# Kernel optimization log

Hardware: AMD Instinct MI355X
Metric: run time of the kernel (lower is better)

Reference implementation:

```python
import jax, jax.numpy as jnp
import numpy as np

N, E, G = 50000, 800000, 512
IN_DIM, EDGE_DIM, HID, OUT_DIM, HEADS = 16, 8, 32, 64, 4
NEG_SLOPE = 0.2


def _glorot(key, shape):
    fan_in, fan_out = shape[0], shape[-1]
    lim = jnp.sqrt(6.0 / (fan_in + fan_out))
    return jax.random.uniform(key, shape, jnp.float32, -lim, lim)


def setup_inputs() -> dict:
    key = jax.random.key(0)
    ks = jax.random.split(key, 32)
    inp = {
        "x": jax.random.normal(ks[0], (N, IN_DIM), jnp.float32),
        "edge_src": jax.random.randint(ks[1], (E,), 0, N, jnp.int32),
        "edge_dst": jax.random.randint(ks[2], (E,), 0, N, jnp.int32),
        "edge_attr": jax.random.normal(ks[3], (E, EDGE_DIM), jnp.float32),
        "batch": jnp.sort(jax.random.randint(ks[4], (N,), 0, G, jnp.int32)),
    }
    # layer 1: in=16 -> heads=4, C=32
    inp["W1s"] = _glorot(ks[5], (IN_DIM, HEADS * HID)); inp["W1d"] = _glorot(ks[6], (IN_DIM, HEADS * HID))
    inp["W1e"] = _glorot(ks[7], (EDGE_DIM, HEADS * HID))
    inp["b1s"] = jnp.zeros((HEADS * HID,)); inp["b1d"] = jnp.zeros((HEADS * HID,))
    inp["att1"] = _glorot(ks[8], (HEADS, HID)); inp["bias1"] = jnp.zeros((HEADS * HID,))
    # layer 2: in=128 -> heads=4, C=32
    D2 = HEADS * HID
    inp["W2s"] = _glorot(ks[9], (D2, HEADS * HID)); inp["W2d"] = _glorot(ks[10], (D2, HEADS * HID))
    inp["W2e"] = _glorot(ks[11], (EDGE_DIM, HEADS * HID))
    inp["b2s"] = jnp.zeros((HEADS * HID,)); inp["b2d"] = jnp.zeros((HEADS * HID,))
    inp["att2"] = _glorot(ks[12], (HEADS, HID)); inp["bias2"] = jnp.zeros((HEADS * HID,))
    # layer 3: in=128 -> heads=1, C=32
    inp["W3s"] = _glorot(ks[13], (D2, HID)); inp["W3d"] = _glorot(ks[14], (D2, HID))
    inp["W3e"] = _glorot(ks[15], (EDGE_DIM, HID))
    inp["b3s"] = jnp.zeros((HID,)); inp["b3d"] = jnp.zeros((HID,))
    inp["att3"] = _glorot(ks[16], (1, HID)); inp["bias3"] = jnp.zeros((HID,))
    # MLP: 32 -> 64 -> 64
    inp["Wm1"] = _glorot(ks[17], (HID, 2 * HID)); inp["bm1"] = jnp.zeros((2 * HID,))
    inp["Wm2"] = _glorot(ks[18], (2 * HID, OUT_DIM)); inp["bm2"] = jnp.zeros((OUT_DIM,))
    return inp


def gatv2_conv(x, src, dst, edge_attr, Ws, Wd, We, bs, bd, att, bias, heads, ch):
    n = x.shape[0]
    xs = (x @ Ws + bs).reshape(n, heads, ch)   # lin_l (source / value)
    xd = (x @ Wd + bd).reshape(n, heads, ch)   # lin_r (target)
    ea = (edge_attr @ We).reshape(-1, heads, ch)
    z = jax.nn.leaky_relu(xs[src] + xd[dst] + ea, NEG_SLOPE)       # [E,H,C]
    e = jnp.einsum('ehc,hc->eh', z, att)                           # [E,H]
    m = jax.ops.segment_max(e, dst, num_segments=n)                # scatter-softmax over dst
    p = jnp.exp(e - m[dst])
    denom = jax.ops.segment_sum(p, dst, num_segments=n)
    alpha = p / denom[dst]                                          # [E,H]
    msg = xs[src] * alpha[:, :, None]                               # [E,H,C]
    out = jax.ops.segment_sum(msg, dst, num_segments=n)
    return out.reshape(n, heads * ch) + bias


def reference(x, edge_src, edge_dst, edge_attr, batch,
              W1s, W1d, W1e, b1s, b1d, att1, bias1,
              W2s, W2d, W2e, b2s, b2d, att2, bias2,
              W3s, W3d, W3e, b3s, b3d, att3, bias3,
              Wm1, bm1, Wm2, bm2):
    h = jax.nn.elu(gatv2_conv(x, edge_src, edge_dst, edge_attr, W1s, W1d, W1e, b1s, b1d, att1, bias1, HEADS, HID))
    h = jax.nn.elu(gatv2_conv(h, edge_src, edge_dst, edge_attr, W2s, W2d, W2e, b2s, b2d, att2, bias2, HEADS, HID))
    h = gatv2_conv(h, edge_src, edge_dst, edge_attr, W3s, W3d, W3e, b3s, b3d, att3, bias3, 1, HID)
    # global mean pool over graphs
    sums = jax.ops.segment_sum(h, batch, num_segments=G)
    cnt = jax.ops.segment_sum(jnp.ones((h.shape[0],), h.dtype), batch, num_segments=G)
    emb = sums / jnp.maximum(cnt, 1.0)[:, None]
    return jax.nn.relu(emb @ Wm1 + bm1) @ Wm2 + bm2
```

## Files before the change

### kernel.cpp

```cpp
#include <hip/hip_runtime.h>
#include <cstdint>
#include <cstddef>

constexpr int kN = 50000;
constexpr int kE = 800000;
constexpr int kG = 512;
constexpr float kNegSlope = 0.2f;

typedef float f4v __attribute__((ext_vector_type(4)));
typedef _Float16 h2v __attribute__((ext_vector_type(2)));
typedef _Float16 h4v __attribute__((ext_vector_type(4)));
typedef _Float16 h8v __attribute__((ext_vector_type(8)));

#if defined(__has_builtin)
#if __has_builtin(__builtin_amdgcn_fdot2)
#define HAS_FDOT2 1
#endif
#endif

__device__ inline float dot2f(h2v a, h2v b, float c) {
#ifdef HAS_FDOT2
  return __builtin_amdgcn_fdot2(a, b, c, false);
#else
  return c + (float)a.x * (float)b.x + (float)a.y * (float)b.y;
#endif
}

__global__ void k_hist(const int* __restrict__ dst, int* __restrict__ counts,
                       int* __restrict__ pos, int n) {
  int i = blockIdx.x * blockDim.x + threadIdx.x;
  if (i < n) pos[i] = atomicAdd(&counts[dst[i]], 1);
}

__global__ __launch_bounds__(256) void k_scan_blk(const int* __restrict__ counts,
                                                  int* __restrict__ excl,
                                                  int* __restrict__ bsums, int n) {
  __shared__ int sh[256];
  int tid = threadIdx.x;
  int i = blockIdx.x * 256 + tid;
  int c = (i < n) ? counts[i] : 0;
  sh[tid] = c;
  __syncthreads();
  for (int off = 1; off < 256; off <<= 1) {
    int t = (tid >= off) ? sh[tid - off] : 0;
    __syncthreads();
    sh[tid] += t;
    __syncthreads();
  }
  if (i < n) excl[i] = sh[tid] - c;
  if (tid == 255) bsums[blockIdx.x] = sh[255];
}

__global__ __launch_bounds__(256) void k_scan_add(const int* __restrict__ excl,
                                                  const int* __restrict__ bsums,
                                                  int* __restrict__ row_ptr,
                                                  int n, int nb) {
  __shared__ int sh[256];
  int tid = threadIdx.x;
  int c = (tid < nb) ? bsums[tid] : 0;
  sh[tid] = c;
  __syncthreads();
  for (int off = 1; off < 256; off <<= 1) {
    int t = (tid >= off) ? sh[tid - off] : 0;
    __syncthreads();
    sh[tid] += t;
    __syncthreads();
  }
  int top = (blockIdx.x > 0) ? sh[blockIdx.x - 1] : 0;
  int total = sh[nb - 1];
  __syncthreads();
  int i = blockIdx.x * 256 + tid;
  if (i < n) row_ptr[i] = excl[i] + top;
  if (i == n) row_ptr[n] = total;
}

__global__ void k_scatter(const int* __restrict__ src, const int* __restrict__ dst,
                          const float* __restrict__ eattr,
                          const int* __restrict__ row_ptr, const int* __restrict__ pos,
                          uint16_t* __restrict__ csr_src, _Float16* __restrict__ csr_ea,
                          int n) {
  int i = blockIdx.x * blockDim.x + threadIdx.x;
  if (i >= n) return;
  int p = row_ptr[dst[i]] + pos[i];
  csr_src[p] = (uint16_t)src[i];
  const float4* s4 = (const float4*)eattr + (size_t)i * 2;
  float4 a = s4[0];
  float4 b = s4[1];
  h8v hv;
  hv[0] = (_Float16)a.x; hv[1] = (_Float16)a.y; hv[2] = (_Float16)a.z; hv[3] = (_Float16)a.w;
  hv[4] = (_Float16)b.x; hv[5] = (_Float16)b.y; hv[6] = (_Float16)b.z; hv[7] = (_Float16)b.w;
  *(h8v*)(csr_ea + (size_t)p * 8) = hv;
}

__global__ __launch_bounds__(256) void k_prep(
    const float* __restrict__ x,
    const float* __restrict__ W1s, const float* __restrict__ W1d,
    const float* __restrict__ W2s, const float* __restrict__ W2d,
    const float* __restrict__ W3s, const float* __restrict__ W3d,
    const float* __restrict__ W1e, const float* __restrict__ W2e,
    const float* __restrict__ W3e,
    int* __restrict__ counts,
    _Float16* __restrict__ xf, _Float16* __restrict__ Wt1,
    _Float16* __restrict__ Wt2, _Float16* __restrict__ Wt3,
    _Float16* __restrict__ We1t, _Float16* __restrict__ We2t,
    _Float16* __restrict__ We3t, int n) {
  int i = blockIdx.x * 256 + threadIdx.x;
  if (i < n) {
    counts[i] = 0;
  }
  i -= n;
  if (i < 0) return;
  int r0 = n * 32;
  if (i < r0) {
    int node = i >> 5, col = i & 31;
    xf[i] = (col < 16) ? (_Float16)x[node * 16 + col] : (_Float16)0.f;
    return;
  }
  i -= r0;
  if (i < 256 * 32) {
    int c = i >> 5, k = i & 31;
    const float* W = (c < 128) ? W1s : W1d;
    Wt1[i] = (k < 16) ? (_Float16)W[k * 128 + (c & 127)] : (_Float16)0.f;
    return;
  }
  i -= 256 * 32;
  if (i < 256 * 128) {
    int c = i >> 7, k = i & 127;
    const float* W = (c < 128) ? W2s : W2d;
    Wt2[i] = (_Float16)W[k * 128 + (c & 127)];
    return;
  }
  i -= 256 * 128;
  if (i < 64 * 128) {
    int c = i >> 7, k = i & 127;
    const float* W = (c < 32) ? W3s : W3d;
    int cc = (c < 32) ? c : c - 32;
    Wt3[i] = (_Float16)W[k * 32 + cc];
    return;
  }
  i -= 64 * 128;
  if (i < 128 * 8) {
    We1t[i] = (_Float16)W1e[(i & 7) * 128 + (i >> 3)];
    return;
  }
  i -= 128 * 8;
  if (i < 128 * 8) {
    We2t[i] = (_Float16)W2e[(i & 7) * 128 + (i >> 3)];
    return;
  }
  i -= 128 * 8;
  if (i < 32 * 8) {
    We3t[i] = (_Float16)W3e[(i & 7) * 32 + (i >> 3)];
  }
}

template <int KT, int NC2>
__global__ __launch_bounds__(256) void k_tmfma(
    const _Float16* __restrict__ hf, const _Float16* __restrict__ Wt,
    const float* __restrict__ bs, const float* __restrict__ bd,
    _Float16* __restrict__ xs_h, _Float16* __restrict__ xd_h, int n_nodes) {
  constexpr int K = KT * 32;
  constexpr int NCS = NC2 / 2;
  constexpr int D = NCS * 16;
  int lane = threadIdx.x & 63;
  int wid = threadIdx.x >> 6;
  int m = lane & 15;
  int quad = lane >> 4;
  int base = (blockIdx.x * 4 + wid) * 16;
  if (base >= n_nodes) return;
  int arow = min(base + m, n_nodes - 1);

  h8v a[KT];
#pragma unroll
  for (int t = 0; t < KT; ++t)
    a[t] = *(const h8v*)(hf + (size_t)arow * K + t * 32 + quad * 8);

  bool full = (base + 16 <= n_nodes);
#pragma unroll
  for (int c = 0; c < NC2; ++c) {
    f4v acc = {0.f, 0.f, 0.f, 0.f};
#pragma unroll
    for (int t = 0; t < KT; ++t) {
      h8v b = *(const h8v*)(Wt + (size_t)(c * 16 + m) * K + t * 32 + quad * 8);
      acc = __builtin_amdgcn_mfma_f32_16x16x32_f16(a[t], b, acc, 0, 0, 0);
    }
    float bv = (c < NCS) ? bs[c * 16 + m] : bd[(c - NCS) * 16 + m];
#pragma unroll
    for (int r = 0; r < 4; ++r) {
      int node = base + quad * 4 + r;
      if (full || node < n_nodes) {
        if (c < NCS)
          xs_h[(size_t)node * D + c * 16 + m] = (_Float16)(acc[r] + bv);
        else
          xd_h[(size_t)node * D + (c - NCS) * 16 + m] = (_Float16)(acc[r] + bv);
      }
    }
  }
}

template <bool DO_ELU>
__global__ __launch_bounds__(64) void k_gat128(
    const int* __restrict__ row_ptr, const uint16_t* __restrict__ csr_src,
    const _Float16* __restrict__ csr_ea,
    const _Float16* __restrict__ xs_h, const _Float16* __restrict__ xd_h,
    const float* __restrict__ att, const float* __restrict__ bias,
    const _Float16* __restrict__ Wet, _Float16* __restrict__ hout, int n_nodes) {
  __shared__ _Float16 sea[64 * 8];
  int lane = threadIdx.x & 63;
  int node = blockIdx.x;
  if (node >= n_nodes) return;
  int slot = lane >> 5;
  int sl = lane & 31;
  int ch0 = sl * 4;

  float4 at4 = *(const float4*)(att + ch0);
  float atl[4] = {at4.x, at4.y, at4.z, at4.w};
  h2v we[4][4];
#pragma unroll
  for (int c = 0; c < 4; ++c) {
    h8v wv = *(const h8v*)(Wet + (size_t)(ch0 + c) * 8);
#pragma unroll
    for (int t = 0; t < 4; ++t) {
      h2v w;
      w[0] = wv[2 * t];
      w[1] = wv[2 * t + 1];
      we[c][t] = w;
    }
  }
  float4 bv4 = *(const float4*)(bias + ch0);
  float bl[4] = {bv4.x, bv4.y, bv4.z, bv4.w};

  h4v xdh = *(const h4v*)(xd_h + (size_t)node * 128 + ch0);
  float xdl[4];
#pragma unroll
  for (int c = 0; c < 4; ++c) xdl[c] = (float)xdh[c];

  const char* xsb = (const char*)xs_h;
  uint32_t chb = (uint32_t)sl * 8u;

  float acc[4] = {0.f, 0.f, 0.f, 0.f};
  float l_run = 0.f;
  int beg = row_ptr[node], end = row_ptr[node + 1];

  for (int cbeg = beg; cbeg < end; cbeg += 64) {
    int cnt = min(end - cbeg, 64);
    int sv = (lane < cnt) ? (int)__builtin_nontemporal_load(csr_src + cbeg + lane) : 0;
    if (lane < cnt) {
      h8v t = __builtin_nontemporal_load((const h8v*)(csr_ea + (size_t)(cbeg + lane) * 8));
      *(h8v*)&sea[lane * 8] = t;
    }

    auto addr = [&](int i) -> uint32_t {
      int s = __shfl(sv, i + slot, 64);
      return (uint32_t)s * 256u + chb;
    };
    auto consume = [&](int i, h4v xh) {
      int e = i + slot;
      const h2v* pe = (const h2v*)&sea[e * 8];
      h2v a0 = pe[0], a1 = pe[1], a2 = pe[2], a3 = pe[3];
      float xf[4];
#pragma unroll
      for (int c = 0; c < 4; ++c) xf[c] = (float)xh[c];
      float sc = 0.f;
#pragma unroll
      for (int c = 0; c < 4; ++c) {
        float z = dot2f(a3, we[c][3],
                  dot2f(a2, we[c][2],
                  dot2f(a1, we[c][1],
                  dot2f(a0, we[c][0], xf[c] + xdl[c]))));
        z = fmaxf(z, kNegSlope * z);
        sc = fmaf(z, atl[c], sc);
      }
      sc += __shfl_xor(sc, 1, 64);
      sc += __shfl_xor(sc, 2, 64);
      sc += __shfl_xor(sc, 4, 64);
      float p = (e < cnt) ? __expf(sc) : 0.f;
      l_run += p;
#pragma unroll
      for (int c = 0; c < 4; ++c) acc[c] += p * xf[c];
    };

    uint32_t oa = addr(0), ob = addr(2);
    h4v xa = *(const h4v*)(xsb + oa);
    h4v xb = *(const h4v*)(xsb + ob);
    for (int i = 0; i < cnt; i += 4) {
      bool pf = (i + 4 < cnt);
      h4v pa, pb;
      if (pf) {
        uint32_t na = addr(i + 4), nb = addr(i + 6);
        pa = *(const h4v*)(xsb + na);
        pb = *(const h4v*)(xsb + nb);
      }
      consume(i, xa);
      consume(i + 2, xb);
      if (pf) { xa = pa; xb = pb; }
    }
  }

  l_run += __shfl_xor(l_run, 32, 64);
#pragma unroll
  for (int c = 0; c < 4; ++c) acc[c] += __shfl_xor(acc[c], 32, 64);

  if (slot == 0) {
    float inv = (l_run > 0.f) ? (1.f / l_run) : 0.f;
    h4v ov;
#pragma unroll
    for (int c = 0; c < 4; ++c) {
      float o = acc[c] * inv + bl[c];
      if (DO_ELU) o = (o > 0.f) ? o : (__expf(o) - 1.f);
      ov[c] = (_Float16)o;
    }
    __builtin_nontemporal_store(ov, (h4v*)(hout + (size_t)node * 128 + ch0));
  }
}

template <bool DO_ELU>
__global__ __launch_bounds__(64) void k_gat32(
    const int* __restrict__ row_ptr, const uint16_t* __restrict__ csr_src,
    const _Float16* __restrict__ csr_ea,
    const _Float16* __restrict__ xs_h, const _Float16* __restrict__ xd_h,
    const float* __restrict__ att, const float* __restrict__ bias,
    const _Float16* __restrict__ Wet, _Float16* __restrict__ hout, int n_nodes) {
  __shared__ _Float16 sea[32 * 8];
  int lane = threadIdx.x & 63;
  int node = blockIdx.x;
  if (node >= n_nodes) return;
  int slot = lane >> 3;
  int sl = lane & 7;
  int ch0 = sl * 4;

  float4 at4 = *(const float4*)(att + ch0);
  float atl[4] = {at4.x, at4.y, at4.z, at4.w};
  h2v we[4][4];
#pragma unroll
  for (int c = 0; c < 4; ++c) {
    h8v wv = *(const h8v*)(Wet + (size_t)(ch0 + c) * 8);
#pragma unroll
    for (int t = 0; t < 4; ++t) {
      h2v w;
      w[0] = wv[2 * t];
      w[1] = wv[2 * t + 1];
      we[c][t] = w;
    }
  }
  float4 bv4 = *(const float4*)(bias + ch0);
  float bl[4] = {bv4.x, bv4.y, bv4.z, bv4.w};

  h4v xdh = *(const h4v*)(xd_h + (size_t)node * 32 + ch0);
  float xdl[4];
#pragma unroll
  for (int c = 0; c < 4; ++c) xdl[c] = (float)xdh[c];

  const char* xsb = (const char*)xs_h;
  uint32_t chb = (uint32_t)sl * 8u;

  float acc[4] = {0.f, 0.f, 0.f, 0.f};
  float l_run = 0.f;
  int beg = row_ptr[node], end = row_ptr[node + 1];

  for (int cbeg = beg; cbeg < end; cbeg += 32) {
    int cnt = min(end - cbeg, 32);
    int sv = (lane < cnt) ? (int)__builtin_nontemporal_load(csr_src + cbeg + lane) : 0;
    if (lane < cnt) {
      h8v t = __builtin_nontemporal_load((const h8v*)(csr_ea + (size_t)(cbeg + lane) * 8));
      *(h8v*)&sea[lane * 8] = t;
    }

    auto addr = [&](int i) -> uint32_t {
      int idx = (i + slot) & 31;
      int s = __shfl(sv, idx, 64);
      return (uint32_t)s * 64u + chb;
    };
    auto consume = [&](int i, h4v xh) {
      int e = i + slot;
      const h2v* pe = (const h2v*)&sea[e * 8];
      h2v a0 = pe[0], a1 = pe[1], a2 = pe[2], a3 = pe[3];
      float xf[4];
#pragma unroll
      for (int c = 0; c < 4; ++c) xf[c] = (float)xh[c];
      float sc = 0.f;
#pragma unroll
      for (int c = 0; c < 4; ++c) {
        float z = dot2f(a3, we[c][3],
                  dot2f(a2, we[c][2],
                  dot2f(a1, we[c][1],
                  dot2f(a0, we[c][0], xf[c] + xdl[c]))));
        z = fmaxf(z, kNegSlope * z);
        sc = fmaf(z, atl[c], sc);
      }
      sc += __shfl_xor(sc, 1, 64);
      sc += __shfl_xor(sc, 2, 64);
      sc += __shfl_xor(sc, 4, 64);
      float p = (e < cnt) ? __expf(sc) : 0.f;
      l_run += p;
#pragma unroll
      for (int c = 0; c < 4; ++c) acc[c] += p * xf[c];
    };

    uint32_t oa = addr(0), ob = addr(8);
    h4v xa = *(const h4v*)(xsb + oa);
    h4v xb = *(const h4v*)(xsb + ob);
    for (int i = 0; i < cnt; i += 16) {
      bool pf = (i + 16 < cnt);
      h4v pa, pb;
      if (pf) {
        uint32_t na = addr(i + 16), nb = addr(i + 24);
        pa = *(const h4v*)(xsb + na);
        pb = *(const h4v*)(xsb + nb);
      }
      consume(i, xa);
      consume(i + 8, xb);
      if (pf) { xa = pa; xb = pb; }
    }
  }

#pragma unroll
  for (int off = 8; off < 64; off <<= 1) {
    l_run += __shfl_xor(l_run, off, 64);
#pragma unroll
    for (int c = 0; c < 4; ++c) acc[c] += __shfl_xor(acc[c], off, 64);
  }

  if (slot == 0) {
    float inv = (l_run > 0.f) ? (1.f / l_run) : 0.f;
    h4v ov;
#pragma unroll
    for (int c = 0; c < 4; ++c) {
      float o = acc[c] * inv + bl[c];
      if (DO_ELU) o = (o > 0.f) ? o : (__expf(o) - 1.f);
      ov[c] = (_Float16)o;
    }
    __builtin_nontemporal_store(ov, (h4v*)(hout + (size_t)node * 32 + ch0));
  }
}

__device__ inline int lowerb(const int* a, int n, int v) {
  int lo = 0, hi = n;
  while (lo < hi) {
    int mid = (lo + hi) >> 1;
    if (a[mid] < v) lo = mid + 1; else hi = mid;
  }
  return lo;
}

__global__ __launch_bounds__(64) void k_pool_mlp(
    const _Float16* __restrict__ h3, const int* __restrict__ batch,
    const float* __restrict__ Wm1, const float* __restrict__ bm1,
    const float* __restrict__ Wm2, const float* __restrict__ bm2,
    float* __restrict__ out, int n_nodes) {
  int g = blockIdx.x;
  int t = threadIdx.x;
  int lo = lowerb(batch, n_nodes, g);
  int hi = lowerb(batch, n_nodes, g + 1);
  int c = t & 31, half = t >> 5;
  float sum = 0.f;
  for (int i = lo + half; i < hi; i += 2) sum += (float)h3[(size_t)i * 32 + c];
  sum += __shfl_xor(sum, 32, 64);
  float cnt = (float)(hi - lo);
  float emb = sum / fmaxf(cnt, 1.f);
  __shared__ float sh_emb[32];
  __shared__ float sh_hid[64];
  if (half == 0) sh_emb[c] = emb;
  __syncthreads();
  float hv = bm1[t];
  for (int k = 0; k < 32; ++k) hv += sh_emb[k] * Wm1[k * 64 + t];
  hv = fmaxf(hv, 0.f);
  sh_hid[t] = hv;
  __syncthreads();
  float ov = bm2[t];
  for (int k = 0; k < 64; ++k) ov += sh_hid[k] * Wm2[k * 64 + t];
  out[(size_t)g * 64 + t] = ov;
}

extern "C" void kernel_launch(void* const* d_in, const int* in_sizes, int n_in,
                              void* d_out, int out_size, void* d_ws, size_t ws_size,
                              hipStream_t stream) {
  const float* x = (const float*)d_in[0];
  const int* esrc = (const int*)d_in[1];
  const int* edst = (const int*)d_in[2];
  const float* eattr = (const float*)d_in[3];
  const int* batch = (const int*)d_in[4];
  const float* W1s = (const float*)d_in[5];
  const float* W1d = (const float*)d_in[6];
  const float* W1e = (const float*)d_in[7];
  const float* b1s = (const float*)d_in[8];
  const float* b1d = (const float*)d_in[9];
  const float* att1 = (const float*)d_in[10];
  const float* bias1 = (const float*)d_in[11];
  const float* W2s = (const float*)d_in[12];
  const float* W2d = (const float*)d_in[13];
  const float* W2e = (const float*)d_in[14];
  const float* b2s = (const float*)d_in[15];
  const float* b2d = (const float*)d_in[16];
  const float* att2 = (const float*)d_in[17];
  const float* bias2 = (const float*)d_in[18];
  const float* W3s = (const float*)d_in[19];
  const float* W3d = (const float*)d_in[20];
  const float* W3e = (const float*)d_in[21];
  const float* b3s = (const float*)d_in[22];
  const float* b3d = (const float*)d_in[23];
  const float* att3 = (const float*)d_in[24];
  const float* bias3 = (const float*)d_in[25];
  const float* Wm1 = (const float*)d_in[26];
  const float* bm1 = (const float*)d_in[27];
  const float* Wm2 = (const float*)d_in[28];
  const float* bm2 = (const float*)d_in[29];

  constexpr int kNB = (kN + 255) / 256;

  char* p = (char*)d_ws;
  auto take = [&](size_t bytes) {
    char* r = p;
    p += (bytes + 255) & ~(size_t)255;
    return r;
  };
  int* row_ptr = (int*)take((size_t)(kN + 1) * sizeof(int));
  int* counts = (int*)take((size_t)kN * sizeof(int));
  int* pos = (int*)take((size_t)kE * sizeof(int));
  int* excl = (int*)take((size_t)kN * sizeof(int));
  int* bsums = (int*)take((size_t)kNB * sizeof(int));
  uint16_t* csr_src = (uint16_t*)take((size_t)kE * sizeof(uint16_t));
  _Float16* csr_ea = (_Float16*)take((size_t)kE * 8 * sizeof(_Float16));
  _Float16* xf = (_Float16*)take((size_t)kN * 32 * sizeof(_Float16));
  _Float16* Wt1 = (_Float16*)take((size_t)256 * 32 * sizeof(_Float16));
  _Float16* Wt2 = (_Float16*)take((size_t)256 * 128 * sizeof(_Float16));
  _Float16* Wt3 = (_Float16*)take((size_t)64 * 128 * sizeof(_Float16));
  _Float16* We1t = (_Float16*)take((size_t)128 * 8 * sizeof(_Float16));
  _Float16* We2t = (_Float16*)take((size_t)128 * 8 * sizeof(_Float16));
  _Float16* We3t = (_Float16*)take((size_t)32 * 8 * sizeof(_Float16));
  _Float16* xs_h = (_Float16*)take((size_t)kN * 128 * sizeof(_Float16));
  _Float16* xd_h = (_Float16*)take((size_t)kN * 128 * sizeof(_Float16));
  _Float16* hA = (_Float16*)take((size_t)kN * 128 * sizeof(_Float16));
  _Float16* hB = (_Float16*)take((size_t)kN * 128 * sizeof(_Float16));
  _Float16* h3 = (_Float16*)take((size_t)kN * 32 * sizeof(_Float16));

  {
    int prep_total = kN + kN * 32 + 256 * 32 + 256 * 128 + 64 * 128 +
                     128 * 8 + 128 * 8 + 32 * 8;
    k_prep<<<(prep_total + 255) / 256, 256, 0, stream>>>(
        x, W1s, W1d, W2s, W2d, W3s, W3d, W1e, W2e, W3e,
        counts, xf, Wt1, Wt2, Wt3, We1t, We2t, We3t, kN);
  }
  k_hist<<<(kE + 255) / 256, 256, 0, stream>>>(edst, counts, pos, kE);
  k_scan_blk<<<kNB, 256, 0, stream>>>(counts, excl, bsums, kN);
  k_scan_add<<<(kN + 1 + 255) / 256, 256, 0, stream>>>(excl, bsums, row_ptr, kN, kNB);
  k_scatter<<<(kE + 255) / 256, 256, 0, stream>>>(esrc, edst, eattr, row_ptr, pos,
                                                  csr_src, csr_ea, kE);

  constexpr int kTB = (kN + 63) / 64;

  k_tmfma<1, 16><<<kTB, 256, 0, stream>>>(xf, Wt1, b1s, b1d, xs_h, xd_h, kN);
  k_gat128<true><<<kN, 64, 0, stream>>>(row_ptr, csr_src, csr_ea, xs_h, xd_h,
                                        att1, bias1, We1t, hA, kN);
  k_tmfma<4, 16><<<kTB, 256, 0, stream>>>(hA, Wt2, b2s, b2d, xs_h, xd_h, kN);
  k_gat128<true><<<kN, 64, 0, stream>>>(row_ptr, csr_src, csr_ea, xs_h, xd_h,
                                        att2, bias2, We2t, hB, kN);
  k_tmfma<4, 4><<<kTB, 256, 0, stream>>>(hB, Wt3, b3s, b3d, xs_h, xd_h, kN);
  k_gat32<false><<<kN, 64, 0, stream>>>(row_ptr, csr_src, csr_ea, xs_h, xd_h,
                                        att3, bias3, We3t, h3, kN);
  k_pool_mlp<<<kG, 64, 0, stream>>>(h3, batch, Wm1, bm1, Wm2, bm2, (float*)d_out, kN);
}
```

Before: 429.5 us.

## Process two nodes per GAT block with prefetched edges, DPP reductions, exp2

Each GAT aggregation block now handles two destination nodes and loads both nodes' first edge chunks up front, so the second node's edge loads overlap the first node's work. Source addresses are staged in LDS instead of being broadcast with shuffles. The score reduction uses DPP adds, and exp is computed as exp2 with log2e folded into the attention vector. Graph offsets for pooling are built in the prep kernel instead of by binary search. Processing the two nodes one after the other inside a block adds latency per block and may lower occupancy through higher register use.

```diff
diff --git a/kernel.cpp b/kernel.cpp
--- a/kernel.cpp
+++ b/kernel.cpp
@@ -6,6 +6,7 @@
 constexpr int kE = 800000;
 constexpr int kG = 512;
 constexpr float kNegSlope = 0.2f;
+constexpr float kLog2e = 1.4426950408889634f;
 
 typedef float f4v __attribute__((ext_vector_type(4)));
 typedef _Float16 h2v __attribute__((ext_vector_type(2)));
@@ -24,6 +25,13 @@
 #else
   return c + (float)a.x * (float)b.x + (float)a.y * (float)b.y;
 #endif
+}
+
+template <int CTRL>
+__device__ inline float dpp_xadd(float x) {
+  int s = __builtin_bit_cast(int, x);
+  int y = __builtin_amdgcn_update_dpp(s, s, CTRL, 0xF, 0xF, false);
+  return x + __builtin_bit_cast(float, y);
 }
 
 __global__ void k_hist(const int* __restrict__ dst, int* __restrict__ counts,
@@ -99,6 +107,7 @@
     const float* __restrict__ W3s, const float* __restrict__ W3d,
     const float* __restrict__ W1e, const float* __restrict__ W2e,
     const float* __restrict__ W3e,
+    const int* __restrict__ batch, int* __restrict__ gptr,
     int* __restrict__ counts,
     _Float16* __restrict__ xf, _Float16* __restrict__ Wt1,
     _Float16* __restrict__ Wt2, _Float16* __restrict__ Wt3,
@@ -107,6 +116,12 @@
   int i = blockIdx.x * 256 + threadIdx.x;
   if (i < n) {
     counts[i] = 0;
+    int b1 = batch[i];
+    int b0 = (i == 0) ? -1 : batch[i - 1];
+    for (int g = b0 + 1; g <= b1; ++g) gptr[g] = i;
+    if (i == n - 1) {
+      for (int g = b1 + 1; g <= kG; ++g) gptr[g] = n;
+    }
   }
   i -= n;
   if (i < 0) return;
@@ -199,22 +214,49 @@
 }
 
 template <bool DO_ELU>
-__global__ __launch_bounds__(64) void k_gat128(
+__global__ __launch_bounds__(64, 8) void k_gat128(
     const int* __restrict__ row_ptr, const uint16_t* __restrict__ csr_src,
     const _Float16* __restrict__ csr_ea,
     const _Float16* __restrict__ xs_h, const _Float16* __restrict__ xd_h,
     const float* __restrict__ att, const float* __restrict__ bias,
     const _Float16* __restrict__ Wet, _Float16* __restrict__ hout, int n_nodes) {
   __shared__ _Float16 sea[64 * 8];
+  __shared__ uint32_t sad[64];
   int lane = threadIdx.x & 63;
-  int node = blockIdx.x;
-  if (node >= n_nodes) return;
+  int node0 = blockIdx.x * 2;
+  if (node0 >= n_nodes) return;
   int slot = lane >> 5;
   int sl = lane & 31;
   int ch0 = sl * 4;
 
+  int nd1 = min(node0 + 1, n_nodes - 1);
+  int beg0 = row_ptr[node0];
+  int mid = row_ptr[node0 + 1];
+  int end1 = row_ptr[nd1 + 1];
+
+  int cnt0 = min(mid - beg0, 64);
+  int sv0 = 0;
+  h8v ea0;
+#pragma unroll
+  for (int q = 0; q < 8; ++q) ea0[q] = (_Float16)0.f;
+  if (cnt0 > 0) {
+    int idx = beg0 + ((lane < cnt0) ? lane : 0);
+    sv0 = (int)__builtin_nontemporal_load(csr_src + idx);
+    ea0 = __builtin_nontemporal_load((const h8v*)(csr_ea + (size_t)idx * 8));
+  }
+  int pcnt = (node0 + 1 < n_nodes) ? min(end1 - mid, 64) : 0;
+  int sv1 = 0;
+  h8v ea1;
+#pragma unroll
+  for (int q = 0; q < 8; ++q) ea1[q] = (_Float16)0.f;
+  if (pcnt > 0) {
+    int idx = mid + ((lane < pcnt) ? lane : 0);
+    sv1 = (int)__builtin_nontemporal_load(csr_src + idx);
+    ea1 = __builtin_nontemporal_load((const h8v*)(csr_ea + (size_t)idx * 8));
+  }
+
   float4 at4 = *(const float4*)(att + ch0);
-  float atl[4] = {at4.x, at4.y, at4.z, at4.w};
+  float atl[4] = {at4.x * kLog2e, at4.y * kLog2e, at4.z * kLog2e, at4.w * kLog2e};
   h2v we[4][4];
 #pragma unroll
   for (int c = 0; c < 4; ++c) {
@@ -229,108 +271,142 @@
   }
   float4 bv4 = *(const float4*)(bias + ch0);
   float bl[4] = {bv4.x, bv4.y, bv4.z, bv4.w};
-
-  h4v xdh = *(const h4v*)(xd_h + (size_t)node * 128 + ch0);
-  float xdl[4];
-#pragma unroll
-  for (int c = 0; c < 4; ++c) xdl[c] = (float)xdh[c];
+  h4v xdh0 = *(const h4v*)(xd_h + (size_t)node0 * 128 + ch0);
+  h4v xdh1 = *(const h4v*)(xd_h + (size_t)nd1 * 128 + ch0);
 
   const char* xsb = (const char*)xs_h;
   uint32_t chb = (uint32_t)sl * 8u;
-
-  float acc[4] = {0.f, 0.f, 0.f, 0.f};
-  float l_run = 0.f;
-  int beg = row_ptr[node], end = row_ptr[node + 1];
-
-  for (int cbeg = beg; cbeg < end; cbeg += 64) {
-    int cnt = min(end - cbeg, 64);
-    int sv = (lane < cnt) ? (int)__builtin_nontemporal_load(csr_src + cbeg + lane) : 0;
-    if (lane < cnt) {
-      h8v t = __builtin_nontemporal_load((const h8v*)(csr_ea + (size_t)(cbeg + lane) * 8));
-      *(h8v*)&sea[lane * 8] = t;
-    }
-
-    auto addr = [&](int i) -> uint32_t {
-      int s = __shfl(sv, i + slot, 64);
-      return (uint32_t)s * 256u + chb;
-    };
-    auto consume = [&](int i, h4v xh) {
-      int e = i + slot;
-      const h2v* pe = (const h2v*)&sea[e * 8];
-      h2v a0 = pe[0], a1 = pe[1], a2 = pe[2], a3 = pe[3];
-      float xf[4];
-#pragma unroll
-      for (int c = 0; c < 4; ++c) xf[c] = (float)xh[c];
-      float sc = 0.f;
+  const uint32_t* sp = &sad[slot];
+
+  auto run_node = [&](int node, int beg, int end, h4v xdh, int psv, h8v pea) {
+    float xdl[4];
+#pragma unroll
+    for (int c = 0; c < 4; ++c) xdl[c] = (float)xdh[c];
+    float acc[4] = {0.f, 0.f, 0.f, 0.f};
+    float l_run = 0.f;
+    for (int cbeg = beg; cbeg < end; cbeg += 64) {
+      int cnt = min(end - cbeg, 64);
+      int sv;
+      h8v ev;
+      if (cbeg == beg) {
+        sv = psv;
+        ev = pea;
+      } else {
+        int idx = cbeg + ((lane < cnt) ? lane : 0);
+        sv = (int)__builtin_nontemporal_load(csr_src + idx);
+        ev = __builtin_nontemporal_load((const h8v*)(csr_ea + (size_t)idx * 8));
+      }
+      sad[lane] = (lane < cnt) ? ((uint32_t)(uint16_t)sv << 8) : 0u;
+      *(h8v*)&sea[lane * 8] = ev;
+
+      auto consume = [&](int i, h4v xh) {
+        int e = i + slot;
+        const h2v* pe = (const h2v*)&sea[e * 8];
+        h2v a0 = pe[0], a1 = pe[1], a2 = pe[2], a3 = pe[3];
+        float xf[4];
+#pragma unroll
+        for (int c = 0; c < 4; ++c) xf[c] = (float)xh[c];
+        float sc = 0.f;
+#pragma unroll
+        for (int c = 0; c < 4; ++c) {
+          float z = dot2f(a3, we[c][3],
+                    dot2f(a2, we[c][2],
+                    dot2f(a1, we[c][1],
+                    dot2f(a0, we[c][0], xf[c] + xdl[c]))));
+          z = fmaxf(z, kNegSlope * z);
+          sc = fmaf(z, atl[c], sc);
+        }
+        sc = dpp_xadd<0xB1>(sc);
+        sc = dpp_xadd<0x4E>(sc);
+        sc = dpp_xadd<0x141>(sc);
+        float p = (e < cnt) ? exp2f(sc) : 0.f;
+        l_run += p;
+#pragma unroll
+        for (int c = 0; c < 4; ++c) acc[c] += p * xf[c];
+      };
+
+      uint32_t oa = sp[0] + chb, ob = sp[2] + chb;
+      h4v xa = *(const h4v*)(xsb + oa);
+      h4v xb = *(const h4v*)(xsb + ob);
+      for (int i = 0; i < cnt; i += 4) {
+        bool pf = (i + 4 < cnt);
+        h4v pa, pb;
+        if (pf) {
+          uint32_t na = sp[i + 4] + chb, nb = sp[i + 6] + chb;
+          pa = *(const h4v*)(xsb + na);
+          pb = *(const h4v*)(xsb + nb);
+        }
+        consume(i, xa);
+        consume(i + 2, xb);
+        if (pf) { xa = pa; xb = pb; }
+      }
+    }
+
+    l_run += __shfl_xor(l_run, 32, 64);
+#pragma unroll
+    for (int c = 0; c < 4; ++c) acc[c] += __shfl_xor(acc[c], 32, 64);
+
+    if (slot == 0) {
+      float inv = (l_run > 0.f) ? (1.f / l_run) : 0.f;
+      h4v ov;
 #pragma unroll
       for (int c = 0; c < 4; ++c) {
-        float z = dot2f(a3, we[c][3],
-                  dot2f(a2, we[c][2],
-                  dot2f(a1, we[c][1],
-                  dot2f(a0, we[c][0], xf[c] + xdl[c]))));
-        z = fmaxf(z, kNegSlope * z);
-        sc = fmaf(z, atl[c], sc);
+        float o = acc[c] * inv + bl[c];
+        if (DO_ELU) o = (o > 0.f) ? o : (__expf(o) - 1.f);
+        ov[c] = (_Float16)o;
       }
-      sc += __shfl_xor(sc, 1, 64);
-      sc += __shfl_xor(sc, 2, 64);
-      sc += __shfl_xor(sc, 4, 64);
-      float p = (e < cnt) ? __expf(sc) : 0.f;
-      l_run += p;
-#pragma unroll
-      for (int c = 0; c < 4; ++c) acc[c] += p * xf[c];
-    };
-
-    uint32_t oa = addr(0), ob = addr(2);
-    h4v xa = *(const h4v*)(xsb + oa);
-    h4v xb = *(const h4v*)(xsb + ob);
-    for (int i = 0; i < cnt; i += 4) {
-      bool pf = (i + 4 < cnt);
-      h4v pa, pb;
-      if (pf) {
-        uint32_t na = addr(i + 4), nb = addr(i + 6);
-        pa = *(const h4v*)(xsb + na);
-        pb = *(const h4v*)(xsb + nb);
-      }
-      consume(i, xa);
-      consume(i + 2, xb);
-      if (pf) { xa = pa; xb = pb; }
-    }
-  }
-
-  l_run += __shfl_xor(l_run, 32, 64);
-#pragma unroll
-  for (int c = 0; c < 4; ++c) acc[c] += __shfl_xor(acc[c], 32, 64);
-
-  if (slot == 0) {
-    float inv = (l_run > 0.f) ? (1.f / l_run) : 0.f;
-    h4v ov;
-#pragma unroll
-    for (int c = 0; c < 4; ++c) {
-      float o = acc[c] * inv + bl[c];
-      if (DO_ELU) o = (o > 0.f) ? o : (__expf(o) - 1.f);
-      ov[c] = (_Float16)o;
-    }
-    __builtin_nontemporal_store(ov, (h4v*)(hout + (size_t)node * 128 + ch0));
-  }
+      __builtin_nontemporal_store(ov, (h4v*)(hout + (size_t)node * 128 + ch0));
+    }
+  };
+
+  run_node(node0, beg0, mid, xdh0, sv0, ea0);
+  if (node0 + 1 < n_nodes) run_node(node0 + 1, mid, end1, xdh1, sv1, ea1);
 }
 
 template <bool DO_ELU>
-__global__ __launch_bounds__(64) void k_gat32(
+__global__ __launch_bounds__(64, 8) void k_gat32(
     const int* __restrict__ row_ptr, const uint16_t* __restrict__ csr_src,
     const _Float16* __restrict__ csr_ea,
     const _Float16* __restrict__ xs_h, const _Float16* __restrict__ xd_h,
     const float* __restrict__ att, const float* __restrict__ bias,
     const _Float16* __restrict__ Wet, _Float16* __restrict__ hout, int n_nodes) {
-  __shared__ _Float16 sea[32 * 8];
+  __shared__ _Float16 sea[64 * 8];
+  __shared__ uint32_t sad[64];
   int lane = threadIdx.x & 63;
-  int node = blockIdx.x;
-  if (node >= n_nodes) return;
+  int node0 = blockIdx.x * 2;
+  if (node0 >= n_nodes) return;
   int slot = lane >> 3;
   int sl = lane & 7;
   int ch0 = sl * 4;
 
+  int nd1 = min(node0 + 1, n_nodes - 1);
+  int beg0 = row_ptr[node0];
+  int mid = row_ptr[node0 + 1];
+  int end1 = row_ptr[nd1 + 1];
+
+  int cnt0 = min(mid - beg0, 32);
+  int sv0 = 0;
+  h8v ea0;
+#pragma unroll
+  for (int q = 0; q < 8; ++q) ea0[q] = (_Float16)0.f;
+  if (cnt0 > 0) {
+    int idx = beg0 + ((lane < cnt0) ? lane : 0);
+    sv0 = (int)__builtin_nontemporal_load(csr_src + idx);
+    ea0 = __builtin_nontemporal_load((const h8v*)(csr_ea + (size_t)idx * 8));
+  }
+  int pcnt = (node0 + 1 < n_nodes) ? min(end1 - mid, 32) : 0;
+  int sv1 = 0;
+  h8v ea1;
+#pragma unroll
+  for (int q = 0; q < 8; ++q) ea1[q] = (_Float16)0.f;
+  if (pcnt > 0) {
+    int idx = mid + ((lane < pcnt) ? lane : 0);
+    sv1 = (int)__builtin_nontemporal_load(csr_src + idx);
+    ea1 = __builtin_nontemporal_load((const h8v*)(csr_ea + (size_t)idx * 8));
+  }
+
   float4 at4 = *(const float4*)(att + ch0);
-  float atl[4] = {at4.x, at4.y, at4.z, at4.w};
+  float atl[4] = {at4.x * kLog2e, at4.y * kLog2e, at4.z * kLog2e, at4.w * kLog2e};
   h2v we[4][4];
 #pragma unroll
   for (int c = 0; c < 4; ++c) {
@@ -345,113 +421,110 @@
   }
   float4 bv4 = *(const float4*)(bias + ch0);
   float bl[4] = {bv4.x, bv4.y, bv4.z, bv4.w};
-
-  h4v xdh = *(const h4v*)(xd_h + (size_t)node * 32 + ch0);
-  float xdl[4];
-#pragma unroll
-  for (int c = 0; c < 4; ++c) xdl[c] = (float)xdh[c];
+  h4v xdh0 = *(const h4v*)(xd_h + (size_t)node0 * 32 + ch0);
+  h4v xdh1 = *(const h4v*)(xd_h + (size_t)nd1 * 32 + ch0);
 
   const char* xsb = (const char*)xs_h;
   uint32_t chb = (uint32_t)sl * 8u;
-
-  float acc[4] = {0.f, 0.f, 0.f, 0.f};
-  float l_run = 0.f;
-  int beg = row_ptr[node], end = row_ptr[node + 1];
-
-  for (int cbeg = beg; cbeg < end; cbeg += 32) {
-    int cnt = min(end - cbeg, 32);
-    int sv = (lane < cnt) ? (int)__builtin_nontemporal_load(csr_src + cbeg + lane) : 0;
-    if (lane < cnt) {
-      h8v t = __builtin_nontemporal_load((const h8v*)(csr_ea + (size_t)(cbeg + lane) * 8));
-      *(h8v*)&sea[lane * 8] = t;
-    }
-
-    auto addr = [&](int i) -> uint32_t {
-      int idx = (i + slot) & 31;
-      int s = __shfl(sv, idx, 64);
-      return (uint32_t)s * 64u + chb;
-    };
-    auto consume = [&](int i, h4v xh) {
-      int e = i + slot;
-      const h2v* pe = (const h2v*)&sea[e * 8];
-      h2v a0 = pe[0], a1 = pe[1], a2 = pe[2], a3 = pe[3];
-      float xf[4];
-#pragma unroll
-      for (int c = 0; c < 4; ++c) xf[c] = (float)xh[c];
-      float sc = 0.f;
+  const uint32_t* sp = &sad[slot];
+
+  auto run_node = [&](int node, int beg, int end, h4v xdh, int psv, h8v pea) {
+    float xdl[4];
+#pragma unroll
+    for (int c = 0; c < 4; ++c) xdl[c] = (float)xdh[c];
+    float acc[4] = {0.f, 0.f, 0.f, 0.f};
+    float l_run = 0.f;
+    for (int cbeg = beg; cbeg < end; cbeg += 32) {
+      int cnt = min(end - cbeg, 32);
+      int sv;
+      h8v ev;
+      if (cbeg == beg) {
+        sv = psv;
+        ev = pea;
+      } else {
+        int idx = cbeg + ((lane < cnt) ? lane : 0);
+        sv = (int)__builtin_nontemporal_load(csr_src + idx);
+        ev = __builtin_nontemporal_load((const h8v*)(csr_ea + (size_t)idx * 8));
+      }
+      sad[lane] = (lane < cnt) ? ((uint32_t)(uint16_t)sv << 6) : 0u;
+      *(h8v*)&sea[lane * 8] = ev;
+
+      auto consume = [&](int i, h4v xh) {
+        int e = i + slot;
+        const h2v* pe = (const h2v*)&sea[e * 8];
+        h2v a0 = pe[0], a1 = pe[1], a2 = pe[2], a3 = pe[3];
+        float xf[4];
+#pragma unroll
+        for (int c = 0; c < 4; ++c) xf[c] = (float)xh[c];
+        float sc = 0.f;
+#pragma unroll
+        for (int c = 0; c < 4; ++c) {
+          float z = dot2f(a3, we[c][3],
+                    dot2f(a2, we[c][2],
+                    dot2f(a1, we[c][1],
+                    dot2f(a0, we[c][0], xf[c] + xdl[c]))));
+          z = fmaxf(z, kNegSlope * z);
+          sc = fmaf(z, atl[c], sc);
+        }
+        sc = dpp_xadd<0xB1>(sc);
+        sc = dpp_xadd<0x4E>(sc);
+        sc = dpp_xadd<0x141>(sc);
+        float p = (e < cnt) ? exp2f(sc) : 0.f;
+        l_run += p;
+#pragma unroll
+        for (int c = 0; c < 4; ++c) acc[c] += p * xf[c];
+      };
+
+      uint32_t oa = sp[0] + chb, ob = sp[8] + chb;
+      h4v xa = *(const h4v*)(xsb + oa);
+      h4v xb = *(const h4v*)(xsb + ob);
+      for (int i = 0; i < cnt; i += 16) {
+        bool pf = (i + 16 < cnt);
+        h4v pa, pb;
+        if (pf) {
+          uint32_t na = sp[i + 16] + chb, nb = sp[i + 24] + chb;
+          pa = *(const h4v*)(xsb + na);
+          pb = *(const h4v*)(xsb + nb);
+        }
+        consume(i, xa);
+        consume(i + 8, xb);
+        if (pf) { xa = pa; xb = pb; }
+      }
+    }
+
+#pragma unroll
+    for (int off = 8; off < 64; off <<= 1) {
+      l_run += __shfl_xor(l_run, off, 64);
+#pragma unroll
+      for (int c = 0; c < 4; ++c) acc[c] += __shfl_xor(acc[c], off, 64);
+    }
+
+    if (slot == 0) {
+      float inv = (l_run > 0.f) ? (1.f / l_run) : 0.f;
+      h4v ov;
 #pragma unroll
       for (int c = 0; c < 4; ++c) {
-        float z = dot2f(a3, we[c][3],
-                  dot2f(a2, we[c][2],
-                  dot2f(a1, we[c][1],
-                  dot2f(a0, we[c][0], xf[c] + xdl[c]))));
-        z = fmaxf(z, kNegSlope * z);
-        sc = fmaf(z, atl[c], sc);
+        float o = acc[c] * inv + bl[c];
+        if (DO_ELU) o = (o > 0.f) ? o : (__expf(o) - 1.f);
+        ov[c] = (_Float16)o;
       }
-      sc += __shfl_xor(sc, 1, 64);
-      sc += __shfl_xor(sc, 2, 64);
-      sc += __shfl_xor(sc, 4, 64);
-      float p = (e < cnt) ? __expf(sc) : 0.f;
-      l_run += p;
-#pragma unroll
-      for (int c = 0; c < 4; ++c) acc[c] += p * xf[c];
-    };
-
-    uint32_t oa = addr(0), ob = addr(8);
-    h4v xa = *(const h4v*)(xsb + oa);
-    h4v xb = *(const h4v*)(xsb + ob);
-    for (int i = 0; i < cnt; i += 16) {
-      bool pf = (i + 16 < cnt);
-      h4v pa, pb;
-      if (pf) {
-        uint32_t na = addr(i + 16), nb = addr(i + 24);
-        pa = *(const h4v*)(xsb + na);
-        pb = *(const h4v*)(xsb + nb);
-      }
-      consume(i, xa);
-      consume(i + 8, xb);
-      if (pf) { xa = pa; xb = pb; }
-    }
-  }
-
-#pragma unroll
-  for (int off = 8; off < 64; off <<= 1) {
-    l_run += __shfl_xor(l_run, off, 64);
-#pragma unroll
-    for (int c = 0; c < 4; ++c) acc[c] += __shfl_xor(acc[c], off, 64);
-  }
-
-  if (slot == 0) {
-    float inv = (l_run > 0.f) ? (1.f / l_run) : 0.f;
-    h4v ov;
-#pragma unroll
-    for (int c = 0; c < 4; ++c) {
-      float o = acc[c] * inv + bl[c];
-      if (DO_ELU) o = (o > 0.f) ? o : (__expf(o) - 1.f);
-      ov[c] = (_Float16)o;
-    }
-    __builtin_nontemporal_store(ov, (h4v*)(hout + (size_t)node * 32 + ch0));
-  }
-}
-
-__device__ inline int lowerb(const int* a, int n, int v) {
-  int lo = 0, hi = n;
-  while (lo < hi) {
-    int mid = (lo + hi) >> 1;
-    if (a[mid] < v) lo = mid + 1; else hi = mid;
-  }
-  return lo;
+      __builtin_nontemporal_store(ov, (h4v*)(hout + (size_t)node * 32 + ch0));
+    }
+  };
+
+  run_node(node0, beg0, mid, xdh0, sv0, ea0);
+  if (node0 + 1 < n_nodes) run_node(node0 + 1, mid, end1, xdh1, sv1, ea1);
 }
 
 __global__ __launch_bounds__(64) void k_pool_mlp(
-    const _Float16* __restrict__ h3, const int* __restrict__ batch,
+    const _Float16* __restrict__ h3, const int* __restrict__ gptr,
     const float* __restrict__ Wm1, const float* __restrict__ bm1,
     const float* __restrict__ Wm2, const float* __restrict__ bm2,
     float* __restrict__ out, int n_nodes) {
   int g = blockIdx.x;
   int t = threadIdx.x;
-  int lo = lowerb(batch, n_nodes, g);
-  int hi = lowerb(batch, n_nodes, g + 1);
+  int lo = gptr[g];
+  int hi = gptr[g + 1];
   int c = t & 31, half = t >> 5;
   float sum = 0.f;
   for (int i = lo + half; i < hi; i += 2) sum += (float)h3[(size_t)i * 32 + c];
@@ -519,6 +592,7 @@
   int* pos = (int*)take((size_t)kE * sizeof(int));
   int* excl = (int*)take((size_t)kN * sizeof(int));
   int* bsums = (int*)take((size_t)kNB * sizeof(int));
+  int* gptr = (int*)take((size_t)(kG + 1) * sizeof(int));
   uint16_t* csr_src = (uint16_t*)take((size_t)kE * sizeof(uint16_t));
   _Float16* csr_ea = (_Float16*)take((size_t)kE * 8 * sizeof(_Float16));
   _Float16* xf = (_Float16*)take((size_t)kN * 32 * sizeof(_Float16));
@@ -539,7 +613,7 @@
                      128 * 8 + 128 * 8 + 32 * 8;
     k_prep<<<(prep_total + 255) / 256, 256, 0, stream>>>(
         x, W1s, W1d, W2s, W2d, W3s, W3d, W1e, W2e, W3e,
-        counts, xf, Wt1, Wt2, Wt3, We1t, We2t, We3t, kN);
+        batch, gptr, counts, xf, Wt1, Wt2, Wt3, We1t, We2t, We3t, kN);
   }
   k_hist<<<(kE + 255) / 256, 256, 0, stream>>>(edst, counts, pos, kE);
   k_scan_blk<<<kNB, 256, 0, stream>>>(counts, excl, bsums, kN);
@@ -548,15 +622,16 @@
                                                   csr_src, csr_ea, kE);
 
   constexpr int kTB = (kN + 63) / 64;
+  constexpr int kGB = (kN + 1) / 2;
 
   k_tmfma<1, 16><<<kTB, 256, 0, stream>>>(xf, Wt1, b1s, b1d, xs_h, xd_h, kN);
-  k_gat128<true><<<kN, 64, 0, stream>>>(row_ptr, csr_src, csr_ea, xs_h, xd_h,
-                                        att1, bias1, We1t, hA, kN);
+  k_gat128<true><<<kGB, 64, 0, stream>>>(row_ptr, csr_src, csr_ea, xs_h, xd_h,
+                                         att1, bias1, We1t, hA, kN);
   k_tmfma<4, 16><<<kTB, 256, 0, stream>>>(hA, Wt2, b2s, b2d, xs_h, xd_h, kN);
-  k_gat128<true><<<kN, 64, 0, stream>>>(row_ptr, csr_src, csr_ea, xs_h, xd_h,
-                                        att2, bias2, We2t, hB, kN);
+  k_gat128<true><<<kGB, 64, 0, stream>>>(row_ptr, csr_src, csr_ea, xs_h, xd_h,
+                                         att2, bias2, We2t, hB, kN);
   k_tmfma<4, 4><<<kTB, 256, 0, stream>>>(hB, Wt3, b3s, b3d, xs_h, xd_h, kN);
-  k_gat32<false><<<kN, 64, 0, stream>>>(row_ptr, csr_src, csr_ea, xs_h, xd_h,
-                                        att3, bias3, We3t, h3, kN);
-  k_pool_mlp<<<kG, 64, 0, stream>>>(h3, batch, Wm1, bm1, Wm2, bm2, (float*)d_out, kN);
-}
+  k_gat32<false><<<kGB, 64, 0, stream>>>(row_ptr, csr_src, csr_ea, xs_h, xd_h,
+                                         att3, bias3, We3t, h3, kN);
+  k_pool_mlp<<<kG, 64, 0, stream>>>(h3, gptr, Wm1, bm1, Wm2, bm2, (float*)d_out, kN);
+}
```

Measured after the change: 466.3 us. 8.6% more time.
